# Kernel optimization log

Measured on AMD Instinct MI355X. Metric: run time of the kernel, lower is better.

## Reference

```python
import jax, jax.numpy as jnp
from jax import lax
import numpy as np
import math

ALPHA = 1000.0
BETA = 100.0
K = 24
INIT_DIM = 64
STAGES = 4
NUM_POINTS = 2048
B = 16
EPS = 1e-5


def embedding_spe(x, out_dim):
    # x: [..., in_dim] -> [..., out_dim] sinusoidal embedding
    in_dim = x.shape[-1]
    feat_dim = math.ceil(out_dim / (in_dim * 2))
    dim_embed = jnp.asarray(ALPHA ** (np.arange(feat_dim) / feat_dim), x.dtype)
    feat_num = feat_dim * 2 * in_dim
    out_idx = np.linspace(0, feat_num - 1, out_dim).astype(np.int64)
    div = BETA * x[..., None] / dim_embed            # [..., in_dim, feat_dim]
    pe = jnp.stack([jnp.sin(div), jnp.cos(div)], -1)  # [..., in_dim, feat_dim, 2]
    pe = pe.reshape(x.shape[:-1] + (feat_num,))       # order matches torch cat(flatten(stack))
    return pe[..., out_idx]


def fps_single(xyz, npoint):
    # xyz: [N,3] -> indices [npoint] (deterministic start at index 0)
    n = xyz.shape[0]

    def body(carry, _):
        dist, farthest = carry
        centroid = xyz[farthest]
        d = jnp.sum((xyz - centroid) ** 2, -1)
        dist = jnp.minimum(dist, d)
        nxt = jnp.argmax(dist).astype(jnp.int32)
        return (dist, nxt), farthest

    init = (jnp.full((n,), 1e10, xyz.dtype), jnp.array(0, jnp.int32))
    _, idx = lax.scan(body, init, None, length=npoint)
    return idx


def knn(k, xyz, new_xyz):
    # xyz [B,N,3], new_xyz [B,S,3] -> [B,S,k] indices of k nearest points
    d = (jnp.sum(new_xyz ** 2, -1, keepdims=True)
         + jnp.sum(xyz ** 2, -1)[:, None, :]
         - 2.0 * jnp.einsum('bsc,bnc->bsn', new_xyz, xyz))
    _, idx = lax.top_k(-d, k)
    return idx


def gather(pts, idx):
    # pts [B,N,C], idx [B,...] -> [B,...,C]
    b = pts.shape[0]
    bi = jnp.arange(b).reshape((b,) + (1,) * (idx.ndim - 1))
    return pts[bi, idx]


def stage(xyz, feat, npoint, out_dim, gamma, beta_p):
    fps_idx = jax.vmap(lambda p: fps_single(p, npoint))(lax.stop_gradient(xyz))
    xyz_s = gather(xyz, fps_idx)    # [B,S,3]
    feat_s = gather(feat, fps_idx)  # [B,S,C]
    idx_knn = knn(K, lax.stop_gradient(xyz), lax.stop_gradient(xyz_s))  # [B,S,K]
    xyz_knn = gather(xyz, idx_knn)    # [B,S,K,3]
    feat_knn = gather(feat, idx_knn)  # [B,S,K,C]
    # normalize by global (unbiased) std, like torch.std over whole tensor
    xyz_c = xyz_knn - xyz_s[:, :, None, :]
    xyz_knn = xyz_c / (jnp.std(xyz_c, ddof=1) + 1e-05)
    feat_c = feat_knn - feat_s[:, :, None, :]
    feat_knn = feat_c / (jnp.std(feat_c, ddof=1) + 1e-05)
    bsz, s, k, c = feat_knn.shape
    feat_knn = jnp.concatenate(
        [feat_knn, jnp.broadcast_to(feat_s[:, :, None, :], (bsz, s, k, c))], -1)  # [B,S,K,2C]
    # SPE aggregation
    pe = embedding_spe(xyz_knn, out_dim)
    w = (feat_knn + pe) * pe
    # neighbor pooling: max + mean over K
    agg = jnp.max(w, -2) + jnp.mean(w, -2)  # [B,S,out_dim]
    # BatchNorm1d (training-mode batch stats, biased var) + exact GELU
    mean = jnp.mean(agg, axis=(0, 1))
    var = jnp.var(agg, axis=(0, 1))
    y = gamma * (agg - mean) / jnp.sqrt(var + EPS) + beta_p
    return xyz_s, jax.nn.gelu(y, approximate=False)


def setup_inputs() -> dict:
    key = jax.random.key(0)
    ks = jax.random.split(key, 2)
    inp = {'xyz': jax.random.normal(ks[0], (B, NUM_POINTS, 3), jnp.float32)}
    dim = INIT_DIM
    for i in range(STAGES):
        dim *= 2
        inp[f'gamma{i}'] = jnp.ones((dim,), jnp.float32)
        inp[f'beta{i}'] = jnp.zeros((dim,), jnp.float32)
    return inp


def reference(xyz, gamma0, beta0, gamma1, beta1, gamma2, beta2, gamma3, beta3):
    gammas = [gamma0, gamma1, gamma2, gamma3]
    betas = [beta0, beta1, beta2, beta3]
    feat = embedding_spe(xyz, INIT_DIM)
    npoint, dim = NUM_POINTS, INIT_DIM
    for i in range(STAGES):
        dim *= 2
        npoint //= 2
        xyz, feat = stage(xyz, feat, npoint, dim, gammas[i], betas[i])
    return jnp.max(feat, -2) + jnp.mean(feat, -2)  # [B, 1024]
```

## Files before the change

kernel.cpp:

```cpp
#include <hip/hip_runtime.h>
#include <math.h>

#pragma clang fp contract(off)

static constexpr int BATCH = 16;
static constexpr int NPTS0 = 2048;
static constexpr int KNN = 24;

static constexpr size_t OFF_STATS = 0;
static constexpr size_t OFF_BN    = 256;
static constexpr size_t OFF_DE    = 32768;
static constexpr size_t OFF_MAP   = 36864;
static constexpr size_t OFF_XYZ1  = 49152;
static constexpr size_t OFF_XYZ2  = OFF_XYZ1 + (size_t)16*1024*3*4;
static constexpr size_t OFF_XYZ3  = OFF_XYZ2 + (size_t)16*512*3*4;
static constexpr size_t OFF_XYZ4  = OFF_XYZ3 + (size_t)16*256*3*4;
static constexpr size_t OFF_FPS0  = OFF_XYZ4 + (size_t)16*128*3*4;
static constexpr size_t OFF_FPS1  = OFF_FPS0 + (size_t)16*1024*4;
static constexpr size_t OFF_FPS2  = OFF_FPS1 + (size_t)16*512*4;
static constexpr size_t OFF_FPS3  = OFF_FPS2 + (size_t)16*256*4;
static constexpr size_t OFF_KNN   = OFF_FPS3 + (size_t)16*128*4;
static constexpr size_t OFF_FEATA = OFF_KNN + (size_t)16*1024*24*4;
static constexpr size_t OFF_FEATB = OFF_FEATA + (size_t)16*2048*64*4;
static constexpr size_t OFF_FEATS = OFF_FEATB + (size_t)16*2048*64*4;
static constexpr size_t OFF_AGG   = OFF_FEATS + (size_t)16*1024*64*4;
static constexpr size_t WS_NEED   = OFF_AGG + (size_t)16*1024*128*4;

__device__ inline uint64_t kmax64(uint64_t a, uint64_t b) { return a > b ? a : b; }

template <int CTRL>
__device__ inline uint64_t dpp_shift64(uint64_t k) {
  int hi = (int)(unsigned)(k >> 32), lo = (int)(unsigned)k;
  int oh = __builtin_amdgcn_update_dpp(hi, hi, CTRL, 0xF, 0xF, false);
  int ol = __builtin_amdgcn_update_dpp(lo, lo, CTRL, 0xF, 0xF, false);
  return ((uint64_t)(unsigned)oh << 32) | (unsigned)ol;
}
__device__ inline uint64_t wave_reduce_max64(uint64_t k) {
  k = kmax64(k, dpp_shift64<0x111>(k));
  k = kmax64(k, dpp_shift64<0x112>(k));
  k = kmax64(k, dpp_shift64<0x114>(k));
  k = kmax64(k, dpp_shift64<0x118>(k));
  k = kmax64(k, dpp_shift64<0x142>(k));
  k = kmax64(k, dpp_shift64<0x143>(k));
  return k;
}

__device__ inline unsigned sortable_f32(float f) {
  unsigned b = __float_as_uint(f);
  unsigned m = (unsigned)((int)b >> 31) | 0x80000000u;
  return b ^ m;
}

__device__ inline unsigned med3u(unsigned a, unsigned b, unsigned c) {
  unsigned r;
  asm("v_med3_u32 %0, %1, %2, %3" : "=v"(r) : "v"(a), "v"(b), "v"(c));
  return r;
}

__device__ inline void ins24(unsigned kk[KNN], unsigned v) {
#pragma unroll
  for (int e = KNN - 1; e >= 1; --e) kk[e] = med3u(kk[e - 1], kk[e], v);
  kk[0] = kk[0] < v ? kk[0] : v;
}

__global__ void init_tables(float* __restrict__ de, int* __restrict__ mp) {
  const int outs[5] = {64, 128, 256, 512, 1024};
  const int fds[5]  = {11, 22, 43, 86, 171};
  const int deo[5]  = {0, 11, 33, 76, 162};
  const int mpo[5]  = {0, 64, 192, 448, 960};
  const int tid = threadIdx.x;
  for (int c = 0; c < 5; ++c) {
    const int fd = fds[c], out = outs[c];
    for (int j = tid; j < fd; j += blockDim.x)
      de[deo[c] + j] = (float)pow(1000.0, (double)j / (double)fd);
    const double step = (double)(6 * fd - 1) / (double)(out - 1);
    for (int f = tid; f < out; f += blockDim.x)
      mp[mpo[c] + f] = (int)(step * (double)f);
  }
}

__global__ __launch_bounds__(256) void embed_init(const float* __restrict__ xyz,
                                                  float* __restrict__ feat,
                                                  const float* __restrict__ de,
                                                  const int* __restrict__ mp) {
  int g = blockIdx.x * blockDim.x + threadIdx.x;
  if (g >= BATCH * NPTS0 * 64) return;
  int c = g & 63;
  int bn = g >> 6;
  int m = mp[c];
  int sc = m & 1;
  int a = m >> 1;
  int ci = a / 11;
  int j = a - ci * 11;
  float x = xyz[bn * 3 + ci];
  float ang = (100.0f * x) / de[j];
  feat[g] = sc ? cosf(ang) : sinf(ang);
}

template <int PTS>
__device__ void fps_stage(const float* lds_cur, float* lds_next,
                          int* __restrict__ fps_idx, float* __restrict__ xyz_next,
                          uint64_t* red) {
  const int S = PTS * 128;
  const int tid = threadIdx.x;
  __syncthreads();
  float px[PTS], py[PTS], pz[PTS], dist[PTS];
  const unsigned nl = ~(unsigned)tid;
#pragma unroll
  for (int p = 0; p < PTS; ++p) {
    int gi = tid + p * 256;
    px[p] = lds_cur[3 * gi];
    py[p] = lds_cur[3 * gi + 1];
    pz[p] = lds_cur[3 * gi + 2];
    dist[p] = 1e10f;
  }
  unsigned sel = 0;
  if (tid == 0) {
    fps_idx[0] = 0;
    float a = lds_cur[0], b = lds_cur[1], c = lds_cur[2];
    xyz_next[0] = a; xyz_next[1] = b; xyz_next[2] = c;
    lds_next[0] = a; lds_next[1] = b; lds_next[2] = c;
  }
  for (int t = 1; t < S; ++t) {
    float cx = lds_cur[3 * sel], cy = lds_cur[3 * sel + 1], cz = lds_cur[3 * sel + 2];
    uint64_t kb = 0;
#pragma unroll
    for (int p = 0; p < PTS; ++p) {
      float dx = px[p] - cx, dy = py[p] - cy, dz = pz[p] - cz;
      float dd = dx * dx + dy * dy;
      dd = dd + dz * dz;
      float nd = fminf(dist[p], dd);
      dist[p] = nd;
      uint64_t key = ((uint64_t)__float_as_uint(nd) << 32) | (unsigned)(nl - (unsigned)(p * 256));
      kb = kmax64(kb, key);
    }
    kb = wave_reduce_max64(kb);
    if ((tid & 63) == 63) red[(t & 1) * 4 + (tid >> 6)] = kb;
    __syncthreads();
    uint64_t k0 = red[(t & 1) * 4 + 0], k1 = red[(t & 1) * 4 + 1];
    uint64_t k2 = red[(t & 1) * 4 + 2], k3 = red[(t & 1) * 4 + 3];
    uint64_t km = kmax64(kmax64(k0, k1), kmax64(k2, k3));
    sel = ~(unsigned)km;
    if (tid == 0) {
      fps_idx[t] = (int)sel;
      float a = lds_cur[3 * sel], b = lds_cur[3 * sel + 1], c = lds_cur[3 * sel + 2];
      xyz_next[3 * t] = a; xyz_next[3 * t + 1] = b; xyz_next[3 * t + 2] = c;
      lds_next[3 * t] = a; lds_next[3 * t + 1] = b; lds_next[3 * t + 2] = c;
    }
  }
}

__global__ __launch_bounds__(256) void fps_all(const float* __restrict__ xyz0,
                                               float* __restrict__ xyz1, float* __restrict__ xyz2,
                                               float* __restrict__ xyz3, float* __restrict__ xyz4,
                                               int* __restrict__ i0, int* __restrict__ i1,
                                               int* __restrict__ i2, int* __restrict__ i3) {
  __shared__ float lds[3 * (2048 + 1024 + 512 + 256 + 128)];
  __shared__ uint64_t red[8];
  const int b = blockIdx.x;
  float* l0 = lds;
  float* l1 = l0 + 3 * 2048;
  float* l2 = l1 + 3 * 1024;
  float* l3 = l2 + 3 * 512;
  float* l4 = l3 + 3 * 256;
  for (int t = threadIdx.x; t < 3 * 2048; t += 256) l0[t] = xyz0[(size_t)b * 3 * 2048 + t];
  fps_stage<8>(l0, l1, i0 + b * 1024, xyz1 + (size_t)b * 1024 * 3, red);
  fps_stage<4>(l1, l2, i1 + b * 512, xyz2 + (size_t)b * 512 * 3, red);
  fps_stage<2>(l2, l3, i2 + b * 256, xyz3 + (size_t)b * 256 * 3, red);
  fps_stage<1>(l3, l4, i3 + b * 128, xyz4 + (size_t)b * 128 * 3, red);
}

static constexpr int MGS = 29;
__global__ __launch_bounds__(256) void knn_tau(const float* __restrict__ db_xyz,
                                               const float* __restrict__ q_xyz,
                                               unsigned* __restrict__ tau,
                                               int Np, int S) {
  extern __shared__ float smem[];
  float4* db = (float4*)smem;
  unsigned* mg = (unsigned*)(db + Np);
  const int tid = threadIdx.x, lane = tid & 63, wv = tid >> 6;
  const int bpb = S >> 6;
  const int b = blockIdx.x / bpb;
  const int qbase = (blockIdx.x % bpb) * 64;
  for (int j = tid; j < Np; j += 256) {
    float x = db_xyz[((size_t)b * Np + j) * 3 + 0];
    float y = db_xyz[((size_t)b * Np + j) * 3 + 1];
    float z = db_xyz[((size_t)b * Np + j) * 3 + 2];
    float pn = x * x + y * y;
    pn = pn + z * z;
    db[j] = make_float4(x, y, z, pn);
  }
  __syncthreads();
  const int s = qbase + lane;
  float qx = q_xyz[((size_t)b * S + s) * 3 + 0];
  float qy = q_xyz[((size_t)b * S + s) * 3 + 1];
  float qz = q_xyz[((size_t)b * S + s) * 3 + 2];
  float qn = qx * qx + qy * qy;
  qn = qn + qz * qz;
  unsigned kk[KNN];
#pragma unroll
  for (int e = 0; e < KNN; ++e) kk[e] = 0xFFFFFFFFu;
  const int cpw = Np >> 2;
  const int beg = wv * cpw, end = beg + cpw;
  for (int j0 = beg; j0 < end; j0 += 8) {
    float4 p[8];
#pragma unroll
    for (int u = 0; u < 8; ++u) p[u] = db[j0 + u];
#pragma unroll
    for (int u = 0; u < 8; ++u) {
      float dot = fmaf(qz, p[u].z, fmaf(qy, p[u].y, qx * p[u].x));
      float d = (qn + p[u].w) - 2.0f * dot;
      unsigned su = sortable_f32(d);
      if (__any(su < kk[KNN - 1])) ins24(kk, su);
    }
  }
  unsigned* myrow = mg + (wv * 64 + lane) * MGS;
#pragma unroll
  for (int e = 0; e < KNN; ++e) myrow[e] = kk[e];
  __syncthreads();
  if (wv == 0) {
    for (int w = 1; w < 4; ++w) {
      const unsigned* orow = mg + (w * 64 + lane) * MGS;
#pragma unroll
      for (int e = 0; e < KNN; ++e) {
        unsigned v = orow[e];
        if (__any(v < kk[KNN - 1])) ins24(kk, v);
      }
    }
    tau[(size_t)b * S + s] = kk[KNN - 1];
  }
}

__global__ __launch_bounds__(256) void knn_collect(const float* __restrict__ db_xyz,
                                                   const float* __restrict__ q_xyz,
                                                   const unsigned* __restrict__ tau,
                                                   int* __restrict__ out_idx,
                                                   int Np, int S) {
  __shared__ uint64_t bufA[4][24];
  __shared__ uint64_t bufB[4][24];
  const int lane = threadIdx.x & 63, wv = threadIdx.x >> 6;
  const int qi = blockIdx.x * 4 + wv;
  const int b = qi / S, s = qi % S;
  float qx = q_xyz[((size_t)b * S + s) * 3 + 0];
  float qy = q_xyz[((size_t)b * S + s) * 3 + 1];
  float qz = q_xyz[((size_t)b * S + s) * 3 + 2];
  float qn = qx * qx + qy * qy;
  qn = qn + qz * qz;
  const unsigned tt = tau[qi];
  int cntA = 0, cntB = 0;
  const unsigned long long lmlt = (1ull << lane) - 1;
  const int iters = Np >> 6;
  for (int it = 0; it < iters; ++it) {
    int j = it * 64 + lane;
    float x = db_xyz[((size_t)b * Np + j) * 3 + 0];
    float y = db_xyz[((size_t)b * Np + j) * 3 + 1];
    float z = db_xyz[((size_t)b * Np + j) * 3 + 2];
    float pn = x * x + y * y;
    pn = pn + z * z;
    float dot = fmaf(qz, z, fmaf(qy, y, qx * x));
    float d = (qn + pn) - 2.0f * dot;
    unsigned su = sortable_f32(d);
    unsigned long long mlt = __ballot(su < tt);
    unsigned long long meq = __ballot(su == tt);
    if (mlt) {
      int pos = cntA + __popcll(mlt & lmlt);
      if (su < tt && pos < 24) bufA[wv][pos] = ((uint64_t)su << 32) | (unsigned)j;
      cntA += __popcll(mlt);
    }
    if (meq) {
      int pos = cntB + __popcll(meq & lmlt);
      if (su == tt && pos < 24) bufB[wv][pos] = ((uint64_t)su << 32) | (unsigned)j;
      cntB += __popcll(meq);
    }
  }
  uint64_t v = (lane < cntA) ? bufA[wv][lane] : ~0ull;
#pragma unroll
  for (int k = 2; k <= 64; k <<= 1) {
#pragma unroll
    for (int m = k >> 1; m > 0; m >>= 1) {
      uint64_t o = __shfl_xor(v, m);
      bool takemin = (((lane & k) == 0) == ((lane & m) == 0));
      uint64_t mn = v < o ? v : o;
      uint64_t mx = v < o ? o : v;
      v = takemin ? mn : mx;
    }
  }
  if (lane < KNN) {
    uint64_t key = (lane < cntA) ? v : bufB[wv][lane - cntA];
    out_idx[(size_t)qi * KNN + lane] = (int)(unsigned)key;
  }
}

__global__ __launch_bounds__(256) void gather_feat_s(const float* __restrict__ feat,
                                                     const int* __restrict__ fidx,
                                                     float* __restrict__ out, int Np, int S, int C) {
  int g = blockIdx.x * blockDim.x + threadIdx.x;
  if (g >= BATCH * S * C) return;
  int c = g % C;
  int bs = g / C;
  int s = bs % S;
  int b = bs / S;
  int src = fidx[b * S + s];
  out[g] = feat[((size_t)b * Np + src) * C + c];
}

__global__ __launch_bounds__(256) void center_reduce(const float* __restrict__ xyz,
                                                     const float* __restrict__ xyz_s,
                                                     const float* __restrict__ feat,
                                                     const float* __restrict__ feat_s,
                                                     const int* __restrict__ kidx,
                                                     double* __restrict__ sums,
                                                     int Np, int S, int C) {
  int g = blockIdx.x * blockDim.x + threadIdx.x;
  int total = BATCH * S * KNN;
  double sx = 0, sxx = 0, sf = 0, sff = 0;
  if (g < total) {
    int bs = g / KNN;
    int s = bs % S;
    int b = bs / S;
    int j = kidx[g];
    const float* pc = xyz + ((size_t)b * Np + j) * 3;
    const float* qc = xyz_s + ((size_t)b * S + s) * 3;
    for (int c = 0; c < 3; ++c) {
      float v = pc[c] - qc[c];
      sx += (double)v;
      sxx += (double)v * (double)v;
    }
    const float4* fr = (const float4*)(feat + ((size_t)b * Np + j) * C);
    const float4* fs = (const float4*)(feat_s + ((size_t)b * S + s) * C);
    for (int c = 0; c < C / 4; ++c) {
      float4 a = fr[c], bq = fs[c];
      float v0 = a.x - bq.x, v1 = a.y - bq.y, v2 = a.z - bq.z, v3 = a.w - bq.w;
      sf += (double)v0 + (double)v1 + (double)v2 + (double)v3;
      sff += (double)v0 * v0 + (double)v1 * v1 + (double)v2 * v2 + (double)v3 * v3;
    }
  }
#pragma unroll
  for (int m = 1; m < 64; m <<= 1) {
    sx += __shfl_xor(sx, m);
    sxx += __shfl_xor(sxx, m);
    sf += __shfl_xor(sf, m);
    sff += __shfl_xor(sff, m);
  }
  __shared__ double part[4][4];
  int wv = threadIdx.x >> 6;
  if ((threadIdx.x & 63) == 0) { part[wv][0] = sx; part[wv][1] = sxx; part[wv][2] = sf; part[wv][3] = sff; }
  __syncthreads();
  if (threadIdx.x == 0) {
    double a = 0, b2 = 0, c2 = 0, d2 = 0;
    for (int w = 0; w < 4; ++w) { a += part[w][0]; b2 += part[w][1]; c2 += part[w][2]; d2 += part[w][3]; }
    atomicAdd(&sums[0], a);
    atomicAdd(&sums[1], b2);
    atomicAdd(&sums[2], c2);
    atomicAdd(&sums[3], d2);
  }
}

template <int CH>
__global__ __launch_bounds__(256) void agg_kernel(const float* __restrict__ xyz,
                                                  const float* __restrict__ xyz_s,
                                                  const float* __restrict__ feat,
                                                  const float* __restrict__ feat_s,
                                                  const int* __restrict__ kidx,
                                                  const double* __restrict__ csums,
                                                  const float* __restrict__ de,
                                                  const int* __restrict__ mp,
                                                  float* __restrict__ agg,
                                                  int Np, int S, int C, int fd,
                                                  double nx_d, double nf_d) {
  const int lane = threadIdx.x & 63;
  const int wv = threadIdx.x >> 6;
  const int q = blockIdx.x * 4 + wv;
  const int s = q % S;
  const int b = q / S;
  double sxd = csums[0], sxxd = csums[1], sfd = csums[2], sffd = csums[3];
  float stdx = sqrtf((float)((sxxd - sxd * sxd / nx_d) / (nx_d - 1.0)));
  float stdf = sqrtf((float)((sffd - sfd * sfd / nf_d) / (nf_d - 1.0)));
  float invx = 1.0f / (stdx + 1e-5f);
  float invf = 1.0f / (stdf + 1e-5f);
  float cx = xyz_s[((size_t)b * S + s) * 3 + 0];
  float cy = xyz_s[((size_t)b * S + s) * 3 + 1];
  float cz = xyz_s[((size_t)b * S + s) * 3 + 2];
  const float* fsrow = feat_s + ((size_t)b * S + s) * C;
  int ci[CH];
  float dev[CH], fsv[CH];
  bool issin[CH], fh[CH];
#pragma unroll
  for (int ch = 0; ch < CH; ++ch) {
    int f = ch * 64 + lane;
    int m = mp[f];
    issin[ch] = (m & 1) == 0;
    int a = m >> 1;
    int cc = a / fd;
    ci[ch] = cc;
    dev[ch] = de[a - cc * fd];
    fh[ch] = f < C;
    fsv[ch] = fh[ch] ? fsrow[f] : fsrow[f - C];
  }
  float wmax[CH], wsum[CH];
#pragma unroll
  for (int ch = 0; ch < CH; ++ch) { wmax[ch] = -3.4e38f; wsum[ch] = 0.f; }
  const int* krow = kidx + ((size_t)b * S + s) * KNN;
  for (int k = 0; k < KNN; ++k) {
    int j = krow[k];
    const float* pr = xyz + ((size_t)b * Np + j) * 3;
    float n0 = (pr[0] - cx) * invx;
    float n1 = (pr[1] - cy) * invx;
    float n2 = (pr[2] - cz) * invx;
    const float* fr = feat + ((size_t)b * Np + j) * C;
#pragma unroll
    for (int ch = 0; ch < CH; ++ch) {
      float xv = (ci[ch] == 0) ? n0 : ((ci[ch] == 1) ? n1 : n2);
      float ang = (100.0f * xv) / dev[ch];
      float sv, cv;
      sincosf(ang, &sv, &cv);
      float pef = issin[ch] ? sv : cv;
      int f = ch * 64 + lane;
      float val = fh[ch] ? (fr[f] - fsv[ch]) * invf : fsv[ch];
      float w = (val + pef) * pef;
      wmax[ch] = fmaxf(wmax[ch], w);
      wsum[ch] += w;
    }
  }
  float* arow = agg + (size_t)q * (CH * 64);
#pragma unroll
  for (int ch = 0; ch < CH; ++ch) {
    int f = ch * 64 + lane;
    arow[f] = wmax[ch] + wsum[ch] / (float)KNN;
  }
}

__global__ __launch_bounds__(256) void bn_reduce(const float* __restrict__ agg,
                                                 double* __restrict__ bns,
                                                 int R, int D) {
  int r0 = blockIdx.x * 64;
  for (int c = threadIdx.x; c < D; c += 256) {
    double s = 0, ss = 0;
    for (int r = 0; r < 64; ++r) {
      float v = agg[(size_t)(r0 + r) * D + c];
      s += (double)v;
      ss += (double)v * (double)v;
    }
    atomicAdd(&bns[c], s);
    atomicAdd(&bns[D + c], ss);
  }
}

__global__ __launch_bounds__(256) void bn_apply(const float* __restrict__ agg,
                                                const double* __restrict__ bns,
                                                const float* __restrict__ gamma,
                                                const float* __restrict__ beta,
                                                float* __restrict__ outf, int R, int D) {
  int g = blockIdx.x * blockDim.x + threadIdx.x;
  if (g >= R * D) return;
  int c = g % D;
  double n = (double)R;
  double mu = bns[c] / n;
  double var = bns[D + c] / n - mu * mu;
  float mean = (float)mu;
  float rstd = 1.0f / sqrtf((float)var + 1e-5f);
  float x = (agg[g] - mean) * rstd;
  float y = gamma[c] * x + beta[c];
  float e = erff(y * 0.70710678118654752440f);
  outf[g] = 0.5f * y * (1.0f + e);
}

__global__ __launch_bounds__(256) void final_kernel(const float* __restrict__ feat,
                                                    float* __restrict__ out) {
  int g = blockIdx.x * blockDim.x + threadIdx.x;
  if (g >= BATCH * 1024) return;
  int f = g % 1024;
  int b = g / 1024;
  const float* base = feat + (size_t)b * 128 * 1024 + f;
  float mx = -3.4e38f;
  float sm = 0.f;
  for (int s = 0; s < 128; ++s) {
    float v = base[(size_t)s * 1024];
    mx = fmaxf(mx, v);
    sm += v;
  }
  out[g] = mx + sm / 128.0f;
}

extern "C" void kernel_launch(void* const* d_in, const int* in_sizes, int n_in,
                              void* d_out, int out_size, void* d_ws, size_t ws_size,
                              hipStream_t stream) {
  (void)in_sizes; (void)n_in; (void)out_size;
  if (ws_size < WS_NEED) return;
  const float* xyz = (const float*)d_in[0];
  const float* gam[4] = {(const float*)d_in[1], (const float*)d_in[3], (const float*)d_in[5], (const float*)d_in[7]};
  const float* bet[4] = {(const float*)d_in[2], (const float*)d_in[4], (const float*)d_in[6], (const float*)d_in[8]};
  char* ws = (char*)d_ws;
  double* stats = (double*)(ws + OFF_STATS);
  double* bns = (double*)(ws + OFF_BN);
  float* de = (float*)(ws + OFF_DE);
  int* mp = (int*)(ws + OFF_MAP);
  float* xyz1 = (float*)(ws + OFF_XYZ1);
  float* xyz2 = (float*)(ws + OFF_XYZ2);
  float* xyz3 = (float*)(ws + OFF_XYZ3);
  float* xyz4 = (float*)(ws + OFF_XYZ4);
  int* fpsI[4] = {(int*)(ws + OFF_FPS0), (int*)(ws + OFF_FPS1), (int*)(ws + OFF_FPS2), (int*)(ws + OFF_FPS3)};
  int* kidx = (int*)(ws + OFF_KNN);
  float* feata = (float*)(ws + OFF_FEATA);
  float* featb = (float*)(ws + OFF_FEATB);
  float* feats = (float*)(ws + OFF_FEATS);
  unsigned* tau = (unsigned*)(ws + OFF_FEATS);
  float* agg = (float*)(ws + OFF_AGG);

  hipMemsetAsync(ws, 0, 32768, stream);
  init_tables<<<1, 256, 0, stream>>>(de, mp);
  fps_all<<<16, 256, 0, stream>>>(xyz, xyz1, xyz2, xyz3, xyz4, fpsI[0], fpsI[1], fpsI[2], fpsI[3]);
  embed_init<<<(BATCH * NPTS0 * 64) / 256, 256, 0, stream>>>(xyz, feata, de, mp);

  const int Ns[4] = {2048, 1024, 512, 256};
  const int Cs[4] = {64, 128, 256, 512};
  const int fdv[4] = {22, 43, 86, 171};
  const int deo[4] = {11, 33, 76, 162};
  const int mpo[4] = {64, 192, 448, 960};
  const float* xin[5] = {xyz, xyz1, xyz2, xyz3, xyz4};
  float* fcur = feata;
  float* fnext = featb;
  int bnoff = 0;
  for (int i = 0; i < 4; ++i) {
    const int Np = Ns[i], S = Np / 2, C = Cs[i], D = 2 * C;
    size_t tau_lds = (size_t)Np * 16 + (size_t)4 * 64 * MGS * 4;
    knn_tau<<<16 * (S / 64), 256, tau_lds, stream>>>(xin[i], xin[i + 1], tau, Np, S);
    knn_collect<<<(BATCH * S) / 4, 256, 0, stream>>>(xin[i], xin[i + 1], tau, kidx, Np, S);
    gather_feat_s<<<(BATCH * S * C) / 256, 256, 0, stream>>>(fcur, fpsI[i], feats, Np, S, C);
    const int tuples = BATCH * S * KNN;
    center_reduce<<<(tuples + 255) / 256, 256, 0, stream>>>(xin[i], xin[i + 1], fcur, feats, kidx,
                                                            stats + 4 * i, Np, S, C);
    double nx = (double)tuples * 3.0;
    double nf = (double)tuples * (double)C;
    dim3 ag((BATCH * S) / 4);
    switch (D / 64) {
      case 2:
        agg_kernel<2><<<ag, 256, 0, stream>>>(xin[i], xin[i + 1], fcur, feats, kidx, stats + 4 * i,
                                              de + deo[i], mp + mpo[i], agg, Np, S, C, fdv[i], nx, nf);
        break;
      case 4:
        agg_kernel<4><<<ag, 256, 0, stream>>>(xin[i], xin[i + 1], fcur, feats, kidx, stats + 4 * i,
                                              de + deo[i], mp + mpo[i], agg, Np, S, C, fdv[i], nx, nf);
        break;
      case 8:
        agg_kernel<8><<<ag, 256, 0, stream>>>(xin[i], xin[i + 1], fcur, feats, kidx, stats + 4 * i,
                                              de + deo[i], mp + mpo[i], agg, Np, S, C, fdv[i], nx, nf);
        break;
      default:
        agg_kernel<16><<<ag, 256, 0, stream>>>(xin[i], xin[i + 1], fcur, feats, kidx, stats + 4 * i,
                                               de + deo[i], mp + mpo[i], agg, Np, S, C, fdv[i], nx, nf);
        break;
    }
    const int R = BATCH * S;
    bn_reduce<<<R / 64, 256, 0, stream>>>(agg, bns + bnoff, R, D);
    bn_apply<<<(R * D) / 256, 256, 0, stream>>>(agg, bns + bnoff, gam[i], bet[i], fnext, R, D);
    bnoff += 2 * D;
    float* t = fcur; fcur = fnext; fnext = t;
  }
  final_kernel<<<(BATCH * 1024) / 256, 256, 0, stream>>>(fcur, (float*)d_out);
}
```

Measured before the change: 1.753 ms.

## Shorten FPS serial loop: per-thread argmax, carry winner coords, buffer outputs in LDS

The farthest-point-sampling loop now finds each thread's best point with a scalar compare before doing a single 64-bit wave reduction. The winning wave publishes the winner's coordinates alongside its key, so every thread takes the next centroid from the reduction row and skips a dependent LDS load by index. Per-iteration global stores of indices and coordinates move into LDS buffers that are flushed once at the end of each stage. This targets latency on the strictly serial critical path of FPS, at the cost of more LDS traffic per step and extra shared memory.

Result: slower. 2.155 ms (+22.9%).

```diff
diff --git a/kernel.cpp b/kernel.cpp
--- a/kernel.cpp
+++ b/kernel.cpp
@@ -98,14 +98,12 @@
 }
 
 template <int PTS>
-__device__ void fps_stage(const float* lds_cur, float* lds_next,
-                          int* __restrict__ fps_idx, float* __restrict__ xyz_next,
-                          uint64_t* red) {
+__device__ void fps_stage(const float* lds_cur, float* lds_next, int* idx_buf,
+                          unsigned* red,
+                          int* __restrict__ fps_idx, float* __restrict__ xyz_next) {
   const int S = PTS * 128;
   const int tid = threadIdx.x;
-  __syncthreads();
   float px[PTS], py[PTS], pz[PTS], dist[PTS];
-  const unsigned nl = ~(unsigned)tid;
 #pragma unroll
   for (int p = 0; p < PTS; ++p) {
     int gi = tid + p * 256;
@@ -114,16 +112,14 @@
     pz[p] = lds_cur[3 * gi + 2];
     dist[p] = 1e10f;
   }
-  unsigned sel = 0;
+  float cx = lds_cur[0], cy = lds_cur[1], cz = lds_cur[2];
   if (tid == 0) {
-    fps_idx[0] = 0;
-    float a = lds_cur[0], b = lds_cur[1], c = lds_cur[2];
-    xyz_next[0] = a; xyz_next[1] = b; xyz_next[2] = c;
-    lds_next[0] = a; lds_next[1] = b; lds_next[2] = c;
+    idx_buf[0] = 0;
+    lds_next[0] = cx; lds_next[1] = cy; lds_next[2] = cz;
   }
   for (int t = 1; t < S; ++t) {
-    float cx = lds_cur[3 * sel], cy = lds_cur[3 * sel + 1], cz = lds_cur[3 * sel + 2];
-    uint64_t kb = 0;
+    float bd = -1.0f;
+    int bp = 0;
 #pragma unroll
     for (int p = 0; p < PTS; ++p) {
       float dx = px[p] - cx, dy = py[p] - cy, dz = pz[p] - cz;
@@ -131,23 +127,54 @@
       dd = dd + dz * dz;
       float nd = fminf(dist[p], dd);
       dist[p] = nd;
-      uint64_t key = ((uint64_t)__float_as_uint(nd) << 32) | (unsigned)(nl - (unsigned)(p * 256));
-      kb = kmax64(kb, key);
-    }
-    kb = wave_reduce_max64(kb);
-    if ((tid & 63) == 63) red[(t & 1) * 4 + (tid >> 6)] = kb;
+      if (nd > bd) { bd = nd; bp = p; }
+    }
+    unsigned gi = (unsigned)tid + ((unsigned)bp << 8);
+    uint64_t key = ((uint64_t)__float_as_uint(bd) << 32) | (~gi);
+    key = wave_reduce_max64(key);
+    unsigned wlo = (unsigned)__builtin_amdgcn_readlane((int)(unsigned)key, 63);
+    unsigned whi = (unsigned)__builtin_amdgcn_readlane((int)(unsigned)(key >> 32), 63);
+    unsigned gi_w = ~wlo;
+    unsigned pw = gi_w >> 8;
+    float wx = px[0], wy = py[0], wz = pz[0];
+#pragma unroll
+    for (int p = 1; p < PTS; ++p)
+      if (pw == (unsigned)p) { wx = px[p]; wy = py[p]; wz = pz[p]; }
+    if (tid == (int)(gi_w & 255u)) {
+      unsigned* row = red + (t & 1) * 32 + (tid >> 6) * 8;
+      row[0] = whi; row[1] = wlo;
+      row[2] = __float_as_uint(wx); row[3] = __float_as_uint(wy); row[4] = __float_as_uint(wz);
+    }
     __syncthreads();
-    uint64_t k0 = red[(t & 1) * 4 + 0], k1 = red[(t & 1) * 4 + 1];
-    uint64_t k2 = red[(t & 1) * 4 + 2], k3 = red[(t & 1) * 4 + 3];
-    uint64_t km = kmax64(kmax64(k0, k1), kmax64(k2, k3));
-    sel = ~(unsigned)km;
+    const unsigned* rp = red + (t & 1) * 32;
+    uint4 q0 = *(const uint4*)(rp + 0);
+    uint4 q1 = *(const uint4*)(rp + 8);
+    uint4 q2 = *(const uint4*)(rp + 16);
+    uint4 q3 = *(const uint4*)(rp + 24);
+    unsigned z0 = rp[4], z1 = rp[12], z2 = rp[20], z3 = rp[28];
+    uint64_t k0 = ((uint64_t)q0.x << 32) | q0.y;
+    uint64_t k1 = ((uint64_t)q1.x << 32) | q1.y;
+    uint64_t k2 = ((uint64_t)q2.x << 32) | q2.y;
+    uint64_t k3 = ((uint64_t)q3.x << 32) | q3.y;
+    bool s01 = k0 >= k1;
+    uint64_t ka = s01 ? k0 : k1;
+    unsigned xa = s01 ? q0.z : q1.z, ya = s01 ? q0.w : q1.w, za = s01 ? z0 : z1;
+    bool s23 = k2 >= k3;
+    uint64_t kb = s23 ? k2 : k3;
+    unsigned xb = s23 ? q2.z : q3.z, yb = s23 ? q2.w : q3.w, zb = s23 ? z2 : z3;
+    bool sab = ka >= kb;
+    uint64_t km = sab ? ka : kb;
+    cx = __uint_as_float(sab ? xa : xb);
+    cy = __uint_as_float(sab ? ya : yb);
+    cz = __uint_as_float(sab ? za : zb);
     if (tid == 0) {
-      fps_idx[t] = (int)sel;
-      float a = lds_cur[3 * sel], b = lds_cur[3 * sel + 1], c = lds_cur[3 * sel + 2];
-      xyz_next[3 * t] = a; xyz_next[3 * t + 1] = b; xyz_next[3 * t + 2] = c;
-      lds_next[3 * t] = a; lds_next[3 * t + 1] = b; lds_next[3 * t + 2] = c;
-    }
-  }
+      idx_buf[t] = (int)(~(unsigned)km);
+      lds_next[3 * t] = cx; lds_next[3 * t + 1] = cy; lds_next[3 * t + 2] = cz;
+    }
+  }
+  __syncthreads();
+  for (int u = tid; u < S; u += 256) fps_idx[u] = idx_buf[u];
+  for (int u = tid; u < 3 * S; u += 256) xyz_next[u] = lds_next[u];
 }
 
 __global__ __launch_bounds__(256) void fps_all(const float* __restrict__ xyz0,
@@ -156,18 +183,24 @@
                                                int* __restrict__ i0, int* __restrict__ i1,
                                                int* __restrict__ i2, int* __restrict__ i3) {
   __shared__ float lds[3 * (2048 + 1024 + 512 + 256 + 128)];
-  __shared__ uint64_t red[8];
+  __shared__ int idxb[1024 + 512 + 256 + 128];
+  __shared__ __align__(16) unsigned red[2 * 4 * 8];
   const int b = blockIdx.x;
   float* l0 = lds;
   float* l1 = l0 + 3 * 2048;
   float* l2 = l1 + 3 * 1024;
   float* l3 = l2 + 3 * 512;
   float* l4 = l3 + 3 * 256;
+  int* ib0 = idxb;
+  int* ib1 = ib0 + 1024;
+  int* ib2 = ib1 + 512;
+  int* ib3 = ib2 + 256;
   for (int t = threadIdx.x; t < 3 * 2048; t += 256) l0[t] = xyz0[(size_t)b * 3 * 2048 + t];
-  fps_stage<8>(l0, l1, i0 + b * 1024, xyz1 + (size_t)b * 1024 * 3, red);
-  fps_stage<4>(l1, l2, i1 + b * 512, xyz2 + (size_t)b * 512 * 3, red);
-  fps_stage<2>(l2, l3, i2 + b * 256, xyz3 + (size_t)b * 256 * 3, red);
-  fps_stage<1>(l3, l4, i3 + b * 128, xyz4 + (size_t)b * 128 * 3, red);
+  __syncthreads();
+  fps_stage<8>(l0, l1, ib0, red, i0 + b * 1024, xyz1 + (size_t)b * 1024 * 3);
+  fps_stage<4>(l1, l2, ib1, red, i1 + b * 512, xyz2 + (size_t)b * 512 * 3);
+  fps_stage<2>(l2, l3, ib2, red, i2 + b * 256, xyz3 + (size_t)b * 256 * 3);
+  fps_stage<1>(l3, l4, ib3, red, i3 + b * 128, xyz4 + (size_t)b * 128 * 3);
 }
 
 static constexpr int MGS = 29;
```

## Fuse KNN threshold, collect, feature gather and center stats into one kernel

Applied to the files above, without the earlier changes.

Merges knn_tau, knn_collect, gather_feat_s and center_reduce into a single knn_center kernel per stage. The per-query tau threshold and the neighbour indices stay in LDS, and center features are read through the FPS index instead of from a gathered copy. embed_init is folded into extra blocks of the FPS kernel so it can run alongside it, and the memset moves into init_tables. The goal is fewer launches and less global traffic. The cost is that each wave now handles 16 queries serially in the collect phase, which reduces parallelism compared with the old one-wave-per-query collect.

After: 1.954 ms. 11.4% more time.

```diff
diff --git a/kernel.cpp b/kernel.cpp
--- a/kernel.cpp
+++ b/kernel.cpp
@@ -22,8 +22,7 @@
 static constexpr size_t OFF_KNN   = OFF_FPS3 + (size_t)16*128*4;
 static constexpr size_t OFF_FEATA = OFF_KNN + (size_t)16*1024*24*4;
 static constexpr size_t OFF_FEATB = OFF_FEATA + (size_t)16*2048*64*4;
-static constexpr size_t OFF_FEATS = OFF_FEATB + (size_t)16*2048*64*4;
-static constexpr size_t OFF_AGG   = OFF_FEATS + (size_t)16*1024*64*4;
+static constexpr size_t OFF_AGG   = OFF_FEATB + (size_t)16*2048*64*4;
 static constexpr size_t WS_NEED   = OFF_AGG + (size_t)16*1024*128*4;
 
 __device__ inline uint64_t kmax64(uint64_t a, uint64_t b) { return a > b ? a : b; }
@@ -63,12 +62,14 @@
   kk[0] = kk[0] < v ? kk[0] : v;
 }
 
-__global__ void init_tables(float* __restrict__ de, int* __restrict__ mp) {
+__global__ void init_tables(float* __restrict__ de, int* __restrict__ mp,
+                            double* __restrict__ zero_region) {
   const int outs[5] = {64, 128, 256, 512, 1024};
   const int fds[5]  = {11, 22, 43, 86, 171};
   const int deo[5]  = {0, 11, 33, 76, 162};
   const int mpo[5]  = {0, 64, 192, 448, 960};
   const int tid = threadIdx.x;
+  for (int u = tid; u < 4096; u += 256) zero_region[u] = 0.0;
   for (int c = 0; c < 5; ++c) {
     const int fd = fds[c], out = outs[c];
     for (int j = tid; j < fd; j += blockDim.x)
@@ -77,24 +78,6 @@
     for (int f = tid; f < out; f += blockDim.x)
       mp[mpo[c] + f] = (int)(step * (double)f);
   }
-}
-
-__global__ __launch_bounds__(256) void embed_init(const float* __restrict__ xyz,
-                                                  float* __restrict__ feat,
-                                                  const float* __restrict__ de,
-                                                  const int* __restrict__ mp) {
-  int g = blockIdx.x * blockDim.x + threadIdx.x;
-  if (g >= BATCH * NPTS0 * 64) return;
-  int c = g & 63;
-  int bn = g >> 6;
-  int m = mp[c];
-  int sc = m & 1;
-  int a = m >> 1;
-  int ci = a / 11;
-  int j = a - ci * 11;
-  float x = xyz[bn * 3 + ci];
-  float ang = (100.0f * x) / de[j];
-  feat[g] = sc ? cosf(ang) : sinf(ang);
 }
 
 template <int PTS>
@@ -150,13 +133,30 @@
   }
 }
 
-__global__ __launch_bounds__(256) void fps_all(const float* __restrict__ xyz0,
-                                               float* __restrict__ xyz1, float* __restrict__ xyz2,
-                                               float* __restrict__ xyz3, float* __restrict__ xyz4,
-                                               int* __restrict__ i0, int* __restrict__ i1,
-                                               int* __restrict__ i2, int* __restrict__ i3) {
+__global__ __launch_bounds__(256) void fps_embed(const float* __restrict__ xyz0,
+                                                 float* __restrict__ xyz1, float* __restrict__ xyz2,
+                                                 float* __restrict__ xyz3, float* __restrict__ xyz4,
+                                                 int* __restrict__ i0, int* __restrict__ i1,
+                                                 int* __restrict__ i2, int* __restrict__ i3,
+                                                 float* __restrict__ feat,
+                                                 const float* __restrict__ de,
+                                                 const int* __restrict__ mp) {
   __shared__ float lds[3 * (2048 + 1024 + 512 + 256 + 128)];
   __shared__ uint64_t red[8];
+  if (blockIdx.x >= 16) {
+    int g = (blockIdx.x - 16) * 256 + threadIdx.x;
+    int c = g & 63;
+    int bn = g >> 6;
+    int m = mp[c];
+    int sc = m & 1;
+    int a = m >> 1;
+    int ci = a / 11;
+    int j = a - ci * 11;
+    float x = xyz0[bn * 3 + ci];
+    float ang = (100.0f * x) / de[j];
+    feat[g] = sc ? cosf(ang) : sinf(ang);
+    return;
+  }
   const int b = blockIdx.x;
   float* l0 = lds;
   float* l1 = l0 + 3 * 2048;
@@ -171,13 +171,23 @@
 }
 
 static constexpr int MGS = 29;
-__global__ __launch_bounds__(256) void knn_tau(const float* __restrict__ db_xyz,
-                                               const float* __restrict__ q_xyz,
-                                               unsigned* __restrict__ tau,
-                                               int Np, int S) {
+template <int CPL>
+__global__ __launch_bounds__(256) void knn_center(const float* __restrict__ db_xyz,
+                                                  const float* __restrict__ q_xyz,
+                                                  const float* __restrict__ feat,
+                                                  const int* __restrict__ fidx,
+                                                  int* __restrict__ out_idx,
+                                                  double* __restrict__ sums,
+                                                  int Np, int S) {
+  const int C = CPL * 64;
   extern __shared__ float smem[];
   float4* db = (float4*)smem;
-  unsigned* mg = (unsigned*)(db + Np);
+  float4* qL = db + Np;
+  unsigned* mg = (unsigned*)(qL + 64);
+  unsigned* tauL = mg + 4 * 64 * MGS;
+  int* kidxL = (int*)(tauL + 64);
+  __shared__ uint64_t bufA[4][24];
+  __shared__ uint64_t bufB[4][24];
   const int tid = threadIdx.x, lane = tid & 63, wv = tid >> 6;
   const int bpb = S >> 6;
   const int b = blockIdx.x / bpb;
@@ -191,12 +201,13 @@
     db[j] = make_float4(x, y, z, pn);
   }
   __syncthreads();
-  const int s = qbase + lane;
-  float qx = q_xyz[((size_t)b * S + s) * 3 + 0];
-  float qy = q_xyz[((size_t)b * S + s) * 3 + 1];
-  float qz = q_xyz[((size_t)b * S + s) * 3 + 2];
+  const int s0 = qbase + lane;
+  float qx = q_xyz[((size_t)b * S + s0) * 3 + 0];
+  float qy = q_xyz[((size_t)b * S + s0) * 3 + 1];
+  float qz = q_xyz[((size_t)b * S + s0) * 3 + 2];
   float qn = qx * qx + qy * qy;
   qn = qn + qz * qz;
+  if (wv == 0) qL[lane] = make_float4(qx, qy, qz, qn);
   unsigned kk[KNN];
 #pragma unroll
   for (int e = 0; e < KNN; ++e) kk[e] = 0xFFFFFFFFu;
@@ -227,112 +238,86 @@
         if (__any(v < kk[KNN - 1])) ins24(kk, v);
       }
     }
-    tau[(size_t)b * S + s] = kk[KNN - 1];
-  }
-}
-
-__global__ __launch_bounds__(256) void knn_collect(const float* __restrict__ db_xyz,
-                                                   const float* __restrict__ q_xyz,
-                                                   const unsigned* __restrict__ tau,
-                                                   int* __restrict__ out_idx,
-                                                   int Np, int S) {
-  __shared__ uint64_t bufA[4][24];
-  __shared__ uint64_t bufB[4][24];
-  const int lane = threadIdx.x & 63, wv = threadIdx.x >> 6;
-  const int qi = blockIdx.x * 4 + wv;
-  const int b = qi / S, s = qi % S;
-  float qx = q_xyz[((size_t)b * S + s) * 3 + 0];
-  float qy = q_xyz[((size_t)b * S + s) * 3 + 1];
-  float qz = q_xyz[((size_t)b * S + s) * 3 + 2];
-  float qn = qx * qx + qy * qy;
-  qn = qn + qz * qz;
-  const unsigned tt = tau[qi];
-  int cntA = 0, cntB = 0;
+    tauL[lane] = kk[KNN - 1];
+  }
+  __syncthreads();
   const unsigned long long lmlt = (1ull << lane) - 1;
   const int iters = Np >> 6;
-  for (int it = 0; it < iters; ++it) {
-    int j = it * 64 + lane;
-    float x = db_xyz[((size_t)b * Np + j) * 3 + 0];
-    float y = db_xyz[((size_t)b * Np + j) * 3 + 1];
-    float z = db_xyz[((size_t)b * Np + j) * 3 + 2];
-    float pn = x * x + y * y;
-    pn = pn + z * z;
-    float dot = fmaf(qz, z, fmaf(qy, y, qx * x));
-    float d = (qn + pn) - 2.0f * dot;
-    unsigned su = sortable_f32(d);
-    unsigned long long mlt = __ballot(su < tt);
-    unsigned long long meq = __ballot(su == tt);
-    if (mlt) {
-      int pos = cntA + __popcll(mlt & lmlt);
-      if (su < tt && pos < 24) bufA[wv][pos] = ((uint64_t)su << 32) | (unsigned)j;
-      cntA += __popcll(mlt);
-    }
-    if (meq) {
-      int pos = cntB + __popcll(meq & lmlt);
-      if (su == tt && pos < 24) bufB[wv][pos] = ((uint64_t)su << 32) | (unsigned)j;
-      cntB += __popcll(meq);
-    }
-  }
-  uint64_t v = (lane < cntA) ? bufA[wv][lane] : ~0ull;
-#pragma unroll
-  for (int k = 2; k <= 64; k <<= 1) {
-#pragma unroll
-    for (int m = k >> 1; m > 0; m >>= 1) {
-      uint64_t o = __shfl_xor(v, m);
-      bool takemin = (((lane & k) == 0) == ((lane & m) == 0));
-      uint64_t mn = v < o ? v : o;
-      uint64_t mx = v < o ? o : v;
-      v = takemin ? mn : mx;
-    }
-  }
-  if (lane < KNN) {
-    uint64_t key = (lane < cntA) ? v : bufB[wv][lane - cntA];
-    out_idx[(size_t)qi * KNN + lane] = (int)(unsigned)key;
-  }
-}
-
-__global__ __launch_bounds__(256) void gather_feat_s(const float* __restrict__ feat,
-                                                     const int* __restrict__ fidx,
-                                                     float* __restrict__ out, int Np, int S, int C) {
-  int g = blockIdx.x * blockDim.x + threadIdx.x;
-  if (g >= BATCH * S * C) return;
-  int c = g % C;
-  int bs = g / C;
-  int s = bs % S;
-  int b = bs / S;
-  int src = fidx[b * S + s];
-  out[g] = feat[((size_t)b * Np + src) * C + c];
-}
-
-__global__ __launch_bounds__(256) void center_reduce(const float* __restrict__ xyz,
-                                                     const float* __restrict__ xyz_s,
-                                                     const float* __restrict__ feat,
-                                                     const float* __restrict__ feat_s,
-                                                     const int* __restrict__ kidx,
-                                                     double* __restrict__ sums,
-                                                     int Np, int S, int C) {
-  int g = blockIdx.x * blockDim.x + threadIdx.x;
-  int total = BATCH * S * KNN;
+  for (int qq = 0; qq < 16; ++qq) {
+    const int q = wv * 16 + qq;
+    const int s = qbase + q;
+    const float4 qv = qL[q];
+    const unsigned tt = tauL[q];
+    int cntA = 0, cntB = 0;
+    for (int it = 0; it < iters; ++it) {
+      int j = it * 64 + lane;
+      float x = db_xyz[((size_t)b * Np + j) * 3 + 0];
+      float y = db_xyz[((size_t)b * Np + j) * 3 + 1];
+      float z = db_xyz[((size_t)b * Np + j) * 3 + 2];
+      float pn = x * x + y * y;
+      pn = pn + z * z;
+      float dot = fmaf(qv.z, z, fmaf(qv.y, y, qv.x * x));
+      float d = (qv.w + pn) - 2.0f * dot;
+      unsigned su = sortable_f32(d);
+      unsigned long long mlt = __ballot(su < tt);
+      unsigned long long meq = __ballot(su == tt);
+      if (mlt) {
+        int pos = cntA + __popcll(mlt & lmlt);
+        if (su < tt && pos < 24) bufA[wv][pos] = ((uint64_t)su << 32) | (unsigned)j;
+        cntA += __popcll(mlt);
+      }
+      if (meq) {
+        int pos = cntB + __popcll(meq & lmlt);
+        if (su == tt && pos < 24) bufB[wv][pos] = ((uint64_t)su << 32) | (unsigned)j;
+        cntB += __popcll(meq);
+      }
+    }
+    uint64_t v = (lane < cntA) ? bufA[wv][lane] : ~0ull;
+#pragma unroll
+    for (int k = 2; k <= 64; k <<= 1) {
+#pragma unroll
+      for (int m = k >> 1; m > 0; m >>= 1) {
+        uint64_t o = __shfl_xor(v, m);
+        bool takemin = (((lane & k) == 0) == ((lane & m) == 0));
+        uint64_t mn = v < o ? v : o;
+        uint64_t mx = v < o ? o : v;
+        v = takemin ? mn : mx;
+      }
+    }
+    if (lane < KNN) {
+      uint64_t key = (lane < cntA) ? v : bufB[wv][lane - cntA];
+      int jj = (int)(unsigned)key;
+      out_idx[((size_t)b * S + s) * KNN + lane] = jj;
+      kidxL[q * KNN + lane] = jj;
+    }
+  }
   double sx = 0, sxx = 0, sf = 0, sff = 0;
-  if (g < total) {
-    int bs = g / KNN;
-    int s = bs % S;
-    int b = bs / S;
-    int j = kidx[g];
-    const float* pc = xyz + ((size_t)b * Np + j) * 3;
-    const float* qc = xyz_s + ((size_t)b * S + s) * 3;
-    for (int c = 0; c < 3; ++c) {
-      float v = pc[c] - qc[c];
-      sx += (double)v;
-      sxx += (double)v * (double)v;
-    }
-    const float4* fr = (const float4*)(feat + ((size_t)b * Np + j) * C);
-    const float4* fs = (const float4*)(feat_s + ((size_t)b * S + s) * C);
-    for (int c = 0; c < C / 4; ++c) {
-      float4 a = fr[c], bq = fs[c];
-      float v0 = a.x - bq.x, v1 = a.y - bq.y, v2 = a.z - bq.z, v3 = a.w - bq.w;
-      sf += (double)v0 + (double)v1 + (double)v2 + (double)v3;
-      sff += (double)v0 * v0 + (double)v1 * v1 + (double)v2 * v2 + (double)v3 * v3;
+  for (int qq = 0; qq < 16; ++qq) {
+    const int q = wv * 16 + qq;
+    const int s = qbase + q;
+    const float4 qv = qL[q];
+    const int src = fidx[b * S + s];
+    const float* fsrow = feat + ((size_t)b * Np + src) * C + lane * CPL;
+    float fsv[CPL];
+#pragma unroll
+    for (int u = 0; u < CPL; ++u) fsv[u] = fsrow[u];
+    if (lane < KNN) {
+      int j = kidxL[q * KNN + lane];
+      float4 p = db[j];
+      float v0 = p.x - qv.x, v1 = p.y - qv.y, v2 = p.z - qv.z;
+      sx += (double)v0 + (double)v1 + (double)v2;
+      sxx += (double)v0 * v0 + (double)v1 * v1 + (double)v2 * v2;
+    }
+#pragma unroll 4
+    for (int k = 0; k < KNN; ++k) {
+      int j = kidxL[q * KNN + k];
+      const float* fr = feat + ((size_t)b * Np + j) * C + lane * CPL;
+#pragma unroll
+      for (int u = 0; u < CPL; ++u) {
+        float v = fr[u] - fsv[u];
+        sf += (double)v;
+        sff += (double)v * (double)v;
+      }
     }
   }
 #pragma unroll
@@ -343,10 +328,9 @@
     sff += __shfl_xor(sff, m);
   }
   __shared__ double part[4][4];
-  int wv = threadIdx.x >> 6;
-  if ((threadIdx.x & 63) == 0) { part[wv][0] = sx; part[wv][1] = sxx; part[wv][2] = sf; part[wv][3] = sff; }
+  if ((tid & 63) == 0) { part[wv][0] = sx; part[wv][1] = sxx; part[wv][2] = sf; part[wv][3] = sff; }
   __syncthreads();
-  if (threadIdx.x == 0) {
+  if (tid == 0) {
     double a = 0, b2 = 0, c2 = 0, d2 = 0;
     for (int w = 0; w < 4; ++w) { a += part[w][0]; b2 += part[w][1]; c2 += part[w][2]; d2 += part[w][3]; }
     atomicAdd(&sums[0], a);
@@ -360,7 +344,7 @@
 __global__ __launch_bounds__(256) void agg_kernel(const float* __restrict__ xyz,
                                                   const float* __restrict__ xyz_s,
                                                   const float* __restrict__ feat,
-                                                  const float* __restrict__ feat_s,
+                                                  const int* __restrict__ fidx,
                                                   const int* __restrict__ kidx,
                                                   const double* __restrict__ csums,
                                                   const float* __restrict__ de,
@@ -381,7 +365,7 @@
   float cx = xyz_s[((size_t)b * S + s) * 3 + 0];
   float cy = xyz_s[((size_t)b * S + s) * 3 + 1];
   float cz = xyz_s[((size_t)b * S + s) * 3 + 2];
-  const float* fsrow = feat_s + ((size_t)b * S + s) * C;
+  const float* fsrow = feat + ((size_t)b * Np + fidx[b * S + s]) * C;
   int ci[CH];
   float dev[CH], fsv[CH];
   bool issin[CH], fh[CH];
@@ -503,14 +487,11 @@
   int* kidx = (int*)(ws + OFF_KNN);
   float* feata = (float*)(ws + OFF_FEATA);
   float* featb = (float*)(ws + OFF_FEATB);
-  float* feats = (float*)(ws + OFF_FEATS);
-  unsigned* tau = (unsigned*)(ws + OFF_FEATS);
   float* agg = (float*)(ws + OFF_AGG);
 
-  hipMemsetAsync(ws, 0, 32768, stream);
-  init_tables<<<1, 256, 0, stream>>>(de, mp);
-  fps_all<<<16, 256, 0, stream>>>(xyz, xyz1, xyz2, xyz3, xyz4, fpsI[0], fpsI[1], fpsI[2], fpsI[3]);
-  embed_init<<<(BATCH * NPTS0 * 64) / 256, 256, 0, stream>>>(xyz, feata, de, mp);
+  init_tables<<<1, 256, 0, stream>>>(de, mp, (double*)ws);
+  fps_embed<<<16 + 8192, 256, 0, stream>>>(xyz, xyz1, xyz2, xyz3, xyz4,
+                                           fpsI[0], fpsI[1], fpsI[2], fpsI[3], feata, de, mp);
 
   const int Ns[4] = {2048, 1024, 512, 256};
   const int Cs[4] = {64, 128, 256, 512};
@@ -523,31 +504,33 @@
   int bnoff = 0;
   for (int i = 0; i < 4; ++i) {
     const int Np = Ns[i], S = Np / 2, C = Cs[i], D = 2 * C;
-    size_t tau_lds = (size_t)Np * 16 + (size_t)4 * 64 * MGS * 4;
-    knn_tau<<<16 * (S / 64), 256, tau_lds, stream>>>(xin[i], xin[i + 1], tau, Np, S);
-    knn_collect<<<(BATCH * S) / 4, 256, 0, stream>>>(xin[i], xin[i + 1], tau, kidx, Np, S);
-    gather_feat_s<<<(BATCH * S * C) / 256, 256, 0, stream>>>(fcur, fpsI[i], feats, Np, S, C);
+    size_t kc_lds = (size_t)Np * 16 + 64 * 16 + (size_t)4 * 64 * MGS * 4 + 64 * 4 + 64 * KNN * 4;
+    dim3 kg(16 * (S / 64));
+    switch (C / 64) {
+      case 1: knn_center<1><<<kg, 256, kc_lds, stream>>>(xin[i], xin[i + 1], fcur, fpsI[i], kidx, stats + 4 * i, Np, S); break;
+      case 2: knn_center<2><<<kg, 256, kc_lds, stream>>>(xin[i], xin[i + 1], fcur, fpsI[i], kidx, stats + 4 * i, Np, S); break;
+      case 4: knn_center<4><<<kg, 256, kc_lds, stream>>>(xin[i], xin[i + 1], fcur, fpsI[i], kidx, stats + 4 * i, Np, S); break;
+      default: knn_center<8><<<kg, 256, kc_lds, stream>>>(xin[i], xin[i + 1], fcur, fpsI[i], kidx, stats + 4 * i, Np, S); break;
+    }
     const int tuples = BATCH * S * KNN;
-    center_reduce<<<(tuples + 255) / 256, 256, 0, stream>>>(xin[i], xin[i + 1], fcur, feats, kidx,
-                                                            stats + 4 * i, Np, S, C);
     double nx = (double)tuples * 3.0;
     double nf = (double)tuples * (double)C;
     dim3 ag((BATCH * S) / 4);
     switch (D / 64) {
       case 2:
-        agg_kernel<2><<<ag, 256, 0, stream>>>(xin[i], xin[i + 1], fcur, feats, kidx, stats + 4 * i,
+        agg_kernel<2><<<ag, 256, 0, stream>>>(xin[i], xin[i + 1], fcur, fpsI[i], kidx, stats + 4 * i,
                                               de + deo[i], mp + mpo[i], agg, Np, S, C, fdv[i], nx, nf);
         break;
       case 4:
-        agg_kernel<4><<<ag, 256, 0, stream>>>(xin[i], xin[i + 1], fcur, feats, kidx, stats + 4 * i,
+        agg_kernel<4><<<ag, 256, 0, stream>>>(xin[i], xin[i + 1], fcur, fpsI[i], kidx, stats + 4 * i,
                                               de + deo[i], mp + mpo[i], agg, Np, S, C, fdv[i], nx, nf);
         break;
       case 8:
-        agg_kernel<8><<<ag, 256, 0, stream>>>(xin[i], xin[i + 1], fcur, feats, kidx, stats + 4 * i,
+        agg_kernel<8><<<ag, 256, 0, stream>>>(xin[i], xin[i + 1], fcur, fpsI[i], kidx, stats + 4 * i,
                                               de + deo[i], mp + mpo[i], agg, Np, S, C, fdv[i], nx, nf);
         break;
       default:
-        agg_kernel<16><<<ag, 256, 0, stream>>>(xin[i], xin[i + 1], fcur, feats, kidx, stats + 4 * i,
+        agg_kernel<16><<<ag, 256, 0, stream>>>(xin[i], xin[i + 1], fcur, fpsI[i], kidx, stats + 4 * i,
                                                de + deo[i], mp + mpo[i], agg, Np, S, C, fdv[i], nx, nf);
         break;
     }
```
